# Performance work log

Measured on AMD Instinct MI355X. Metric: run time of the kernel, lower is better.

## Reference

```python
import jax, jax.numpy as jnp
import numpy as np

INF = 1000000000000000.0  # 1e15, matches the TF source

B, H, S, D = 4, 16, 1024, 64


def setup_inputs() -> dict:
    key = jax.random.key(0)
    kq, kk, kv, kp = jax.random.split(key, 4)
    q = jax.random.normal(kq, (B, H, S, D), dtype=jnp.float32)
    k = jax.random.normal(kk, (B, H, S, D), dtype=jnp.float32)
    v = jax.random.normal(kv, (B, H, S, D), dtype=jnp.float32)
    # pad_mask: 1 = masked-out key position, broadcast over heads and queries
    pad_mask = jax.random.randint(kp, (B, 1, 1, S), 0, 2, dtype=jnp.int32)
    # look_ahead_mask: 1 above the diagonal (future positions masked)
    look_ahead_mask = jnp.triu(jnp.ones((S, S), dtype=jnp.int32), k=1)[None, None]
    return {"q": q, "k": k, "v": v, "pad_mask": pad_mask,
            "look_ahead_mask": look_ahead_mask}


def reference(q, k, v, pad_mask, look_ahead_mask):
    d_model = jnp.float32(q.shape[3])
    # scores: (B, H, Sq, Sk)
    score_logits = jnp.einsum("bhqd,bhkd->bhqk", q, k) / jnp.sqrt(d_model)
    if pad_mask is not None:
        score_logits = score_logits + pad_mask.astype(jnp.float32) * (-INF)
    if look_ahead_mask is not None:
        score_logits = score_logits + look_ahead_mask.astype(jnp.float32) * (-INF)
    attention_weights = jax.nn.softmax(score_logits, axis=-1)
    context_vector = jnp.einsum("bhqk,bhkd->bhqd", attention_weights, v)
    return (context_vector, attention_weights)
```

## Files before the change

kernel.cpp:

```cpp
#include <hip/hip_runtime.h>
#include <stdint.h>

#define S 1024
#define D 64
#define TQ 16
#define KT 128
#define NKT 8
#define NEG (-1e15f)
#define SCALE 0.125f

#define WB_STRIDE 1048
#define QS_STRIDE 72

typedef __bf16 bf16x8 __attribute__((ext_vector_type(8)));
typedef float f32x4 __attribute__((ext_vector_type(4)));
typedef unsigned short ushort_t;

__device__ __forceinline__ unsigned short f2b(float f) {
  union { float f; uint32_t u; } c; c.f = f;
  uint32_t u = c.u;
  return (unsigned short)((u + 0x7fffu + ((u >> 16) & 1u)) >> 16);
}
__device__ __forceinline__ float b2f(uint32_t u) {
  union { uint32_t u; float f; } c; c.u = u << 16;
  return c.f;
}

__global__ __launch_bounds__(256) void prep_k_kernel(
    const float* __restrict__ Kg, ushort_t* __restrict__ Kb)
{
  const size_t idx = ((size_t)blockIdx.x * 256 + threadIdx.x) * 8;
  float4 a = *(const float4*)(Kg + idx);
  float4 b = *(const float4*)(Kg + idx + 4);
  ushort_t tmp[8];
  tmp[0]=f2b(a.x); tmp[1]=f2b(a.y); tmp[2]=f2b(a.z); tmp[3]=f2b(a.w);
  tmp[4]=f2b(b.x); tmp[5]=f2b(b.y); tmp[6]=f2b(b.z); tmp[7]=f2b(b.w);
  *(uint4*)(Kb + idx) = *(const uint4*)tmp;
}

__global__ __launch_bounds__(256) void prep_vt_kernel(
    const float* __restrict__ Vg, ushort_t* __restrict__ Vt)
{
  __shared__ __align__(16) ushort_t lvt[D * QS_STRIDE];
  const int t = threadIdx.x;
  const int bh = blockIdx.x >> 4;
  const int j0 = (blockIdx.x & 15) << 6;

  {
    const int j = t >> 2, sd = (t & 3) << 4;
    const float* src = Vg + ((size_t)bh * S + j0 + j) * D + sd;
#pragma unroll
    for (int c = 0; c < 4; ++c) {
      float4 f = *(const float4*)(src + (c << 2));
      lvt[(sd + (c << 2) + 0) * QS_STRIDE + j] = f2b(f.x);
      lvt[(sd + (c << 2) + 1) * QS_STRIDE + j] = f2b(f.y);
      lvt[(sd + (c << 2) + 2) * QS_STRIDE + j] = f2b(f.z);
      lvt[(sd + (c << 2) + 3) * QS_STRIDE + j] = f2b(f.w);
    }
  }
  __syncthreads();
  {
    const int d = t >> 2, sj = (t & 3) << 4;
    ushort_t tmp[16];
#pragma unroll
    for (int c = 0; c < 4; ++c)
      *(ushort4*)&tmp[c << 2] = *(const ushort4*)&lvt[d * QS_STRIDE + sj + (c << 2)];
    ushort_t* dst = Vt + ((size_t)bh * D + d) * S + j0 + sj;
    *(uint4*)dst = *(const uint4*)&tmp[0];
    *(uint4*)(dst + 8) = *(const uint4*)&tmp[8];
  }
}

__global__ __launch_bounds__(512, 6) void attn_kernel(
    const float* __restrict__ Qg, const ushort_t* __restrict__ Kb,
    const ushort_t* __restrict__ Vtb, const int* __restrict__ PADg,
    float* __restrict__ OCTX, float* __restrict__ OW)
{
  __shared__ __align__(16) ushort_t wb[TQ * WB_STRIDE];

  const int t  = threadIdx.x;
  const int w  = t >> 6;
  const int l  = t & 63;
  const int la = l & 15;
  const int lb = l >> 4;
  const int blk = blockIdx.x;
  const int bh  = blk >> 6;
  const int qt  = blk & 63;
  const int qr0 = qt << 4;

  const size_t head = (size_t)bh * S * D;
  const int* pp = PADg + (size_t)(bh >> 4) * S;

  bf16x8 aq0, aq1;
  {
    const float* qrow = Qg + head + (size_t)(qr0 + la) * D + (lb << 3);
    float4 q00 = *(const float4*)(qrow);
    float4 q01 = *(const float4*)(qrow + 4);
    float4 q10 = *(const float4*)(qrow + 32);
    float4 q11 = *(const float4*)(qrow + 36);
    ushort_t a0[8], a1[8];
    a0[0]=f2b(q00.x); a0[1]=f2b(q00.y); a0[2]=f2b(q00.z); a0[3]=f2b(q00.w);
    a0[4]=f2b(q01.x); a0[5]=f2b(q01.y); a0[6]=f2b(q01.z); a0[7]=f2b(q01.w);
    a1[0]=f2b(q10.x); a1[1]=f2b(q10.y); a1[2]=f2b(q10.z); a1[3]=f2b(q10.w);
    a1[4]=f2b(q11.x); a1[5]=f2b(q11.y); a1[6]=f2b(q11.z); a1[7]=f2b(q11.w);
    aq0 = *(const bf16x8*)a0;
    aq1 = *(const bf16x8*)a1;
  }

  {
    const ushort_t* kcol = Kb + head + (size_t)((w << 4) + la) * D + (lb << 3);
#pragma unroll
    for (int kt = 0; kt < NKT; ++kt) {
      const ushort_t* kr = kcol + (size_t)(kt * KT) * D;
      f32x4 acc = {0.f, 0.f, 0.f, 0.f};
      bf16x8 b0 = *(const bf16x8*)(kr);
      acc = __builtin_amdgcn_mfma_f32_16x16x32_bf16(aq0, b0, acc, 0, 0, 0);
      bf16x8 b1 = *(const bf16x8*)(kr + 32);
      acc = __builtin_amdgcn_mfma_f32_16x16x32_bf16(aq1, b1, acc, 0, 0, 0);
#pragma unroll
      for (int i = 0; i < 4; ++i)
        wb[((lb << 2) + i) * WB_STRIDE + kt * KT + (w << 4) + la] = f2b(acc[i]);
    }
  }
  __syncthreads();

#pragma unroll
  for (int rr = 0; rr < 2; ++rr) {
    const int r  = (w << 1) + rr;
    const int qr = qr0 + r;
    float lg[16];
    float m = -3.0e38f;
#pragma unroll
    for (int ii = 0; ii < 8; ++ii) {
      const int j = (l << 1) + (ii << 7);
      uint32_t pr = *(const uint32_t*)&wb[r * WB_STRIDE + j];
      int2 pv = *(const int2*)&pp[j];
      float l0 = b2f(pr & 0xffffu) * SCALE + (pv.x ? NEG : 0.0f) + ((j     > qr) ? NEG : 0.0f);
      float l1 = b2f(pr >> 16)     * SCALE + (pv.y ? NEG : 0.0f) + ((j + 1 > qr) ? NEG : 0.0f);
      lg[2 * ii] = l0; lg[2 * ii + 1] = l1;
      m = fmaxf(m, fmaxf(l0, l1));
    }
#pragma unroll
    for (int off = 32; off > 0; off >>= 1) m = fmaxf(m, __shfl_xor(m, off, 64));
    float sum = 0.f;
#pragma unroll
    for (int x = 0; x < 16; ++x) { lg[x] = __expf(lg[x] - m); sum += lg[x]; }
#pragma unroll
    for (int off = 32; off > 0; off >>= 1) sum += __shfl_xor(sum, off, 64);
    const float inv = 1.0f / sum;
    float* orow = OW + (size_t)(bh * S + qr) * S;
#pragma unroll
    for (int ii = 0; ii < 8; ++ii) {
      const int j = (l << 1) + (ii << 7);
      float w0 = lg[2 * ii] * inv, w1 = lg[2 * ii + 1] * inv;
      *(uint32_t*)&wb[r * WB_STRIDE + j] = ((uint32_t)f2b(w1) << 16) | (uint32_t)f2b(w0);
      unsigned long long uw = ((unsigned long long)__float_as_uint(w1) << 32)
                            | (unsigned long long)__float_as_uint(w0);
      __builtin_nontemporal_store(uw, (unsigned long long*)&orow[j]);
    }
  }
  __syncthreads();

  const int jh = w >> 2;
  const int d0 = (w & 3) << 4;
  f32x4 cacc = {0.f, 0.f, 0.f, 0.f};
  {
    const ushort_t* vrow = Vtb + (size_t)bh * D * S + (size_t)(d0 + la) * S
                          + jh * 64 + (lb << 3);
#pragma unroll
    for (int kt = 0; kt < NKT; ++kt) {
#pragma unroll
      for (int ks = 0; ks < 2; ++ks) {
        const int jt = jh * 64 + ks * 32;
        bf16x8 af = *(const bf16x8*)&wb[la * WB_STRIDE + kt * KT + jt + (lb << 3)];
        bf16x8 bf = *(const bf16x8*)(vrow + kt * KT + ks * 32);
        cacc = __builtin_amdgcn_mfma_f32_16x16x32_bf16(af, bf, cacc, 0, 0, 0);
      }
    }
  }
  __syncthreads();

  float* pbuf = (float*)wb;
  if (w >= 4) {
#pragma unroll
    for (int i = 0; i < 4; ++i)
      pbuf[(w - 4) * 320 + ((lb << 2) + i) * 20 + la] = cacc[i];
  }
  __syncthreads();
  if (w < 4) {
#pragma unroll
    for (int i = 0; i < 4; ++i) {
      const int qrow = (lb << 2) + i;
      __builtin_nontemporal_store(
          cacc[i] + pbuf[w * 320 + qrow * 20 + la],
          &OCTX[((size_t)(bh * S) + qr0 + qrow) * D + d0 + la]);
    }
  }
}

extern "C" void kernel_launch(void* const* d_in, const int* in_sizes, int n_in,
                              void* d_out, int out_size, void* d_ws, size_t ws_size,
                              hipStream_t stream) {
  const float* q   = (const float*)d_in[0];
  const float* k   = (const float*)d_in[1];
  const float* v   = (const float*)d_in[2];
  const int*   pad = (const int*)d_in[3];
  float* ctx  = (float*)d_out;
  float* wout = (float*)d_out + (size_t)4 * 16 * S * D;

  ushort_t* Kb  = (ushort_t*)d_ws;
  ushort_t* Vtb = (ushort_t*)d_ws + (size_t)4 * 16 * S * D;

  prep_k_kernel <<<dim3(2048), dim3(256), 0, stream>>>(k, Kb);
  prep_vt_kernel<<<dim3(1024), dim3(256), 0, stream>>>(v, Vtb);
  attn_kernel   <<<dim3(4096), dim3(512), 0, stream>>>(q, Kb, Vtb, pad, ctx, wout);
}
```

Before: 437.9 us.

## Remap blocks across heads and software-pipeline K and V loads with dual accumulators

Remaps the block index so consecutive hardware blocks are spread across eight heads, which is meant to change how the XCDs share L2 across K/V data. Adds explicit register prefetching of K fragments three tiles ahead in the QK^T loop. Adds prefetching of V and LDS weight fragments in the PV loop, with two alternating MFMA accumulators to break the dependency chain. The cost is higher register pressure, which could hurt occupancy under the 512x6 launch bounds.

```diff
diff --git a/kernel.cpp b/kernel.cpp
--- a/kernel.cpp
+++ b/kernel.cpp
@@ -83,10 +83,12 @@
   const int l  = t & 63;
   const int la = l & 15;
   const int lb = l >> 4;
-  const int blk = blockIdx.x;
-  const int bh  = blk >> 6;
-  const int qt  = blk & 63;
-  const int qr0 = qt << 4;
+
+  const int hwblk = blockIdx.x;
+  const int slot  = hwblk >> 3;
+  const int bh    = ((hwblk & 7) << 3) + (slot >> 6);
+  const int qt    = slot & 63;
+  const int qr0   = qt << 4;
 
   const size_t head = (size_t)bh * S * D;
   const int* pp = PADg + (size_t)(bh >> 4) * S;
@@ -108,19 +110,26 @@
   }
 
   {
-    const ushort_t* kcol = Kb + head + (size_t)((w << 4) + la) * D + (lb << 3);
+    const ushort_t* kbase = Kb + head + (size_t)((w << 4) + la) * D + (lb << 3);
+    bf16x8 k0[3], k1[3];
+#define LOADK(KTI, SL) do { \
+      const ushort_t* kr_ = kbase + (size_t)((KTI) * KT) * D; \
+      k0[SL] = *(const bf16x8*)(kr_); \
+      k1[SL] = *(const bf16x8*)(kr_ + 32); } while (0)
+    LOADK(0, 0); LOADK(1, 1); LOADK(2, 2);
 #pragma unroll
     for (int kt = 0; kt < NKT; ++kt) {
-      const ushort_t* kr = kcol + (size_t)(kt * KT) * D;
+      const int s = kt % 3;
+      bf16x8 c0 = k0[s], c1 = k1[s];
+      if (kt + 3 < NKT) LOADK(kt + 3, s);
       f32x4 acc = {0.f, 0.f, 0.f, 0.f};
-      bf16x8 b0 = *(const bf16x8*)(kr);
-      acc = __builtin_amdgcn_mfma_f32_16x16x32_bf16(aq0, b0, acc, 0, 0, 0);
-      bf16x8 b1 = *(const bf16x8*)(kr + 32);
-      acc = __builtin_amdgcn_mfma_f32_16x16x32_bf16(aq1, b1, acc, 0, 0, 0);
+      acc = __builtin_amdgcn_mfma_f32_16x16x32_bf16(aq0, c0, acc, 0, 0, 0);
+      acc = __builtin_amdgcn_mfma_f32_16x16x32_bf16(aq1, c1, acc, 0, 0, 0);
 #pragma unroll
       for (int i = 0; i < 4; ++i)
         wb[((lb << 2) + i) * WB_STRIDE + kt * KT + (w << 4) + la] = f2b(acc[i]);
     }
+#undef LOADK
   }
   __syncthreads();
 
@@ -163,20 +172,31 @@
 
   const int jh = w >> 2;
   const int d0 = (w & 3) << 4;
-  f32x4 cacc = {0.f, 0.f, 0.f, 0.f};
+  f32x4 cacc;
   {
     const ushort_t* vrow = Vtb + (size_t)bh * D * S + (size_t)(d0 + la) * S
                           + jh * 64 + (lb << 3);
-#pragma unroll
-    for (int kt = 0; kt < NKT; ++kt) {
-#pragma unroll
-      for (int ks = 0; ks < 2; ++ks) {
-        const int jt = jh * 64 + ks * 32;
-        bf16x8 af = *(const bf16x8*)&wb[la * WB_STRIDE + kt * KT + jt + (lb << 3)];
-        bf16x8 bf = *(const bf16x8*)(vrow + kt * KT + ks * 32);
-        cacc = __builtin_amdgcn_mfma_f32_16x16x32_bf16(af, bf, cacc, 0, 0, 0);
-      }
-    }
+    const ushort_t* wrow = &wb[la * WB_STRIDE + jh * 64 + (lb << 3)];
+    bf16x8 vv[3], aa[2];
+#define LOADV(ST, SL) do { \
+      vv[SL] = *(const bf16x8*)(vrow + ((ST) >> 1) * KT + ((ST) & 1) * 32); } while (0)
+#define LOADA(ST, SL) do { \
+      aa[SL] = *(const bf16x8*)(wrow + ((ST) >> 1) * KT + ((ST) & 1) * 32); } while (0)
+    LOADV(0, 0); LOADV(1, 1); LOADV(2, 2);
+    LOADA(0, 0); LOADA(1, 1);
+    f32x4 ca = {0.f, 0.f, 0.f, 0.f}, cb = {0.f, 0.f, 0.f, 0.f};
+#pragma unroll
+    for (int st = 0; st < 16; ++st) {
+      bf16x8 av = aa[st & 1];
+      bf16x8 bv = vv[st % 3];
+      if (st + 2 < 16) LOADA(st + 2, st & 1);
+      if (st + 3 < 16) LOADV(st + 3, st % 3);
+      if (st & 1) cb = __builtin_amdgcn_mfma_f32_16x16x32_bf16(av, bv, cb, 0, 0, 0);
+      else        ca = __builtin_amdgcn_mfma_f32_16x16x32_bf16(av, bv, ca, 0, 0, 0);
+    }
+    cacc = ca + cb;
+#undef LOADV
+#undef LOADA
   }
   __syncthreads();
 
```

Result: no change. 438.1 us (+0.1%).

## Prefetch K/V fragments into registers, swizzle block order, use LDS-only barriers

Applied to the files above, without the earlier changes.

Loads all K fragments into registers before the QK MFMAs, and issues the V fragment loads before the softmax so their latency overlaps with softmax work. Pad mask values are loaded once into registers instead of once per row. Blocks are remapped so consecutive hardware block IDs are spread across heads. The PV accumulation is split into two independent chains, and __syncthreads is replaced by barriers that wait only on LDS counters, so outstanding global stores are not drained. Holding the prefetched fragments raises register use, and launch bounds drop from 6 to 4 waves per SIMD to make room.

```diff
diff --git a/kernel.cpp b/kernel.cpp
--- a/kernel.cpp
+++ b/kernel.cpp
@@ -24,6 +24,12 @@
 __device__ __forceinline__ float b2f(uint32_t u) {
   union { uint32_t u; float f; } c; c.u = u << 16;
   return c.f;
+}
+
+__device__ __forceinline__ void barrier_lds_only() {
+  asm volatile("s_waitcnt lgkmcnt(0)" ::: "memory");
+  __builtin_amdgcn_s_barrier();
+  __builtin_amdgcn_sched_barrier(0);
 }
 
 __global__ __launch_bounds__(256) void prep_k_kernel(
@@ -71,7 +77,7 @@
   }
 }
 
-__global__ __launch_bounds__(512, 6) void attn_kernel(
+__global__ __launch_bounds__(512, 4) void attn_kernel(
     const float* __restrict__ Qg, const ushort_t* __restrict__ Kb,
     const ushort_t* __restrict__ Vtb, const int* __restrict__ PADg,
     float* __restrict__ OCTX, float* __restrict__ OW)
@@ -83,13 +89,24 @@
   const int l  = t & 63;
   const int la = l & 15;
   const int lb = l >> 4;
-  const int blk = blockIdx.x;
-  const int bh  = blk >> 6;
-  const int qt  = blk & 63;
-  const int qr0 = qt << 4;
+
+  const int hwblk = blockIdx.x;
+  const int slot  = hwblk >> 3;
+  const int bh    = ((hwblk & 7) << 3) + (slot >> 6);
+  const int qt    = slot & 63;
+  const int qr0   = qt << 4;
 
   const size_t head = (size_t)bh * S * D;
   const int* pp = PADg + (size_t)(bh >> 4) * S;
+
+  float padf[16];
+#pragma unroll
+  for (int ii = 0; ii < 8; ++ii) {
+    const int j = (l << 1) + (ii << 7);
+    int2 pv = *(const int2*)&pp[j];
+    padf[2 * ii]     = pv.x ? NEG : 0.0f;
+    padf[2 * ii + 1] = pv.y ? NEG : 0.0f;
+  }
 
   bf16x8 aq0, aq1;
   {
@@ -108,21 +125,33 @@
   }
 
   {
-    const ushort_t* kcol = Kb + head + (size_t)((w << 4) + la) * D + (lb << 3);
+    const ushort_t* kbase = Kb + head + (size_t)((w << 4) + la) * D + (lb << 3);
+    bf16x8 kf[16];
+#pragma unroll
+    for (int st = 0; st < 16; ++st)
+      kf[st] = *(const bf16x8*)(kbase + (size_t)(st >> 1) * (KT * D) + (st & 1) * 32);
+    __builtin_amdgcn_sched_barrier(0);
 #pragma unroll
     for (int kt = 0; kt < NKT; ++kt) {
-      const ushort_t* kr = kcol + (size_t)(kt * KT) * D;
       f32x4 acc = {0.f, 0.f, 0.f, 0.f};
-      bf16x8 b0 = *(const bf16x8*)(kr);
-      acc = __builtin_amdgcn_mfma_f32_16x16x32_bf16(aq0, b0, acc, 0, 0, 0);
-      bf16x8 b1 = *(const bf16x8*)(kr + 32);
-      acc = __builtin_amdgcn_mfma_f32_16x16x32_bf16(aq1, b1, acc, 0, 0, 0);
+      acc = __builtin_amdgcn_mfma_f32_16x16x32_bf16(aq0, kf[2 * kt],     acc, 0, 0, 0);
+      acc = __builtin_amdgcn_mfma_f32_16x16x32_bf16(aq1, kf[2 * kt + 1], acc, 0, 0, 0);
 #pragma unroll
       for (int i = 0; i < 4; ++i)
         wb[((lb << 2) + i) * WB_STRIDE + kt * KT + (w << 4) + la] = f2b(acc[i]);
     }
   }
   __syncthreads();
+
+  const int jh = w >> 2;
+  const int d0 = (w & 3) << 4;
+  const ushort_t* vrow = Vtb + (size_t)bh * (D * S) + (size_t)(d0 + la) * S
+                        + jh * 64 + (lb << 3);
+  bf16x8 vf[16];
+#pragma unroll
+  for (int st = 0; st < 16; ++st)
+    vf[st] = *(const bf16x8*)(vrow + (st >> 1) * KT + (st & 1) * 32);
+  __builtin_amdgcn_sched_barrier(0);
 
 #pragma unroll
   for (int rr = 0; rr < 2; ++rr) {
@@ -134,9 +163,8 @@
     for (int ii = 0; ii < 8; ++ii) {
       const int j = (l << 1) + (ii << 7);
       uint32_t pr = *(const uint32_t*)&wb[r * WB_STRIDE + j];
-      int2 pv = *(const int2*)&pp[j];
-      float l0 = b2f(pr & 0xffffu) * SCALE + (pv.x ? NEG : 0.0f) + ((j     > qr) ? NEG : 0.0f);
-      float l1 = b2f(pr >> 16)     * SCALE + (pv.y ? NEG : 0.0f) + ((j + 1 > qr) ? NEG : 0.0f);
+      float l0 = b2f(pr & 0xffffu) * SCALE + padf[2 * ii]     + ((j     > qr) ? NEG : 0.0f);
+      float l1 = b2f(pr >> 16)     * SCALE + padf[2 * ii + 1] + ((j + 1 > qr) ? NEG : 0.0f);
       lg[2 * ii] = l0; lg[2 * ii + 1] = l1;
       m = fmaxf(m, fmaxf(l0, l1));
     }
@@ -159,26 +187,21 @@
       __builtin_nontemporal_store(uw, (unsigned long long*)&orow[j]);
     }
   }
-  __syncthreads();
-
-  const int jh = w >> 2;
-  const int d0 = (w & 3) << 4;
-  f32x4 cacc = {0.f, 0.f, 0.f, 0.f};
-  {
-    const ushort_t* vrow = Vtb + (size_t)bh * D * S + (size_t)(d0 + la) * S
-                          + jh * 64 + (lb << 3);
-#pragma unroll
-    for (int kt = 0; kt < NKT; ++kt) {
-#pragma unroll
-      for (int ks = 0; ks < 2; ++ks) {
-        const int jt = jh * 64 + ks * 32;
-        bf16x8 af = *(const bf16x8*)&wb[la * WB_STRIDE + kt * KT + jt + (lb << 3)];
-        bf16x8 bf = *(const bf16x8*)(vrow + kt * KT + ks * 32);
-        cacc = __builtin_amdgcn_mfma_f32_16x16x32_bf16(af, bf, cacc, 0, 0, 0);
-      }
-    }
-  }
-  __syncthreads();
+  barrier_lds_only();
+
+  f32x4 cacc;
+  {
+    const ushort_t* wrow = &wb[la * WB_STRIDE + jh * 64 + (lb << 3)];
+    f32x4 ca = {0.f, 0.f, 0.f, 0.f}, cb = {0.f, 0.f, 0.f, 0.f};
+#pragma unroll
+    for (int st = 0; st < 16; ++st) {
+      bf16x8 av = *(const bf16x8*)(wrow + (st >> 1) * KT + (st & 1) * 32);
+      if (st & 1) cb = __builtin_amdgcn_mfma_f32_16x16x32_bf16(av, vf[st], cb, 0, 0, 0);
+      else        ca = __builtin_amdgcn_mfma_f32_16x16x32_bf16(av, vf[st], ca, 0, 0, 0);
+    }
+    cacc = ca + cb;
+  }
+  barrier_lds_only();
 
   float* pbuf = (float*)wb;
   if (w >= 4) {
@@ -186,7 +209,7 @@
     for (int i = 0; i < 4; ++i)
       pbuf[(w - 4) * 320 + ((lb << 2) + i) * 20 + la] = cacc[i];
   }
-  __syncthreads();
+  barrier_lds_only();
   if (w < 4) {
 #pragma unroll
     for (int i = 0; i < 4; ++i) {
```

Measured after the change: 436.3 us. Within noise of the previous version (-0.4%).

## Stage K and V tiles through LDS with register prefetch and XCD-aware block mapping

Applied to the files above, without the earlier changes.

K and V^T tiles are now loaded cooperatively and coalesced into a shared LDS buffer, one tile at a time. The next tile is prefetched into registers while the current tile is consumed by MFMA, replacing per-wave strided global loads. Block indices are remapped so that consecutive hardware blocks, which are spread across XCDs, group heads onto the same XCD to improve L2 reuse of K/V. Barriers wait only on LDS counters, so outstanding global stores and loads are not drained. The cost is extra barriers per tile, more LDS use that may reduce occupancy, and added register pressure.

```diff
diff --git a/kernel.cpp b/kernel.cpp
--- a/kernel.cpp
+++ b/kernel.cpp
@@ -10,6 +10,8 @@
 #define SCALE 0.125f
 
 #define WB_STRIDE 1048
+#define KB_STRIDE 72
+#define VT_STRIDE 136
 #define QS_STRIDE 72
 
 typedef __bf16 bf16x8 __attribute__((ext_vector_type(8)));
@@ -24,6 +26,12 @@
 __device__ __forceinline__ float b2f(uint32_t u) {
   union { uint32_t u; float f; } c; c.u = u << 16;
   return c.f;
+}
+
+__device__ __forceinline__ void barrier_lds_only() {
+  asm volatile("s_waitcnt lgkmcnt(0)" ::: "memory");
+  __builtin_amdgcn_s_barrier();
+  __builtin_amdgcn_sched_barrier(0);
 }
 
 __global__ __launch_bounds__(256) void prep_k_kernel(
@@ -77,16 +85,19 @@
     float* __restrict__ OCTX, float* __restrict__ OW)
 {
   __shared__ __align__(16) ushort_t wb[TQ * WB_STRIDE];
+  __shared__ __align__(16) ushort_t ub[KT * KB_STRIDE];
 
   const int t  = threadIdx.x;
   const int w  = t >> 6;
   const int l  = t & 63;
   const int la = l & 15;
   const int lb = l >> 4;
-  const int blk = blockIdx.x;
-  const int bh  = blk >> 6;
-  const int qt  = blk & 63;
-  const int qr0 = qt << 4;
+
+  const int hwblk = blockIdx.x;
+  const int slot  = hwblk >> 3;
+  const int bh    = ((hwblk & 7) << 3) + (slot >> 6);
+  const int qt    = slot & 63;
+  const int qr0   = qt << 4;
 
   const size_t head = (size_t)bh * S * D;
   const int* pp = PADg + (size_t)(bh >> 4) * S;
@@ -108,21 +119,37 @@
   }
 
   {
-    const ushort_t* kcol = Kb + head + (size_t)((w << 4) + la) * D + (lb << 3);
-#pragma unroll
+    const int krow = t >> 2, koff = (t & 3) << 4;
+    const ushort_t* ksrc = Kb + head + (size_t)krow * D + koff;
+    ushort_t* kdst = &ub[krow * KB_STRIDE + koff];
+    uint4 kra = *(const uint4*)(ksrc);
+    uint4 krb = *(const uint4*)(ksrc + 8);
     for (int kt = 0; kt < NKT; ++kt) {
-      const ushort_t* kr = kcol + (size_t)(kt * KT) * D;
+      *(uint4*)kdst = kra;
+      *(uint4*)(kdst + 8) = krb;
+      barrier_lds_only();
+      if (kt + 1 < NKT) {
+        const ushort_t* nsrc = ksrc + (size_t)(kt + 1) * (KT * D);
+        kra = *(const uint4*)(nsrc);
+        krb = *(const uint4*)(nsrc + 8);
+      }
+      const int j0 = w << 4;
       f32x4 acc = {0.f, 0.f, 0.f, 0.f};
-      bf16x8 b0 = *(const bf16x8*)(kr);
+      bf16x8 b0 = *(const bf16x8*)&ub[(j0 + la) * KB_STRIDE + (lb << 3)];
       acc = __builtin_amdgcn_mfma_f32_16x16x32_bf16(aq0, b0, acc, 0, 0, 0);
-      bf16x8 b1 = *(const bf16x8*)(kr + 32);
+      bf16x8 b1 = *(const bf16x8*)&ub[(j0 + la) * KB_STRIDE + 32 + (lb << 3)];
       acc = __builtin_amdgcn_mfma_f32_16x16x32_bf16(aq1, b1, acc, 0, 0, 0);
 #pragma unroll
       for (int i = 0; i < 4; ++i)
-        wb[((lb << 2) + i) * WB_STRIDE + kt * KT + (w << 4) + la] = f2b(acc[i]);
-    }
-  }
-  __syncthreads();
+        wb[((lb << 2) + i) * WB_STRIDE + kt * KT + j0 + la] = f2b(acc[i]);
+      barrier_lds_only();
+    }
+  }
+
+  const int vrow = t >> 3, voff = (t & 7) << 4;
+  const ushort_t* vsrc = Vtb + (size_t)bh * (D * S) + (size_t)vrow * S + voff;
+  uint4 vra = *(const uint4*)(vsrc);
+  uint4 vrb = *(const uint4*)(vsrc + 8);
 
 #pragma unroll
   for (int rr = 0; rr < 2; ++rr) {
@@ -159,34 +186,38 @@
       __builtin_nontemporal_store(uw, (unsigned long long*)&orow[j]);
     }
   }
-  __syncthreads();
+  barrier_lds_only();
 
   const int jh = w >> 2;
   const int d0 = (w & 3) << 4;
+  ushort_t* vdst = &ub[vrow * VT_STRIDE + voff];
   f32x4 cacc = {0.f, 0.f, 0.f, 0.f};
-  {
-    const ushort_t* vrow = Vtb + (size_t)bh * D * S + (size_t)(d0 + la) * S
-                          + jh * 64 + (lb << 3);
-#pragma unroll
-    for (int kt = 0; kt < NKT; ++kt) {
-#pragma unroll
-      for (int ks = 0; ks < 2; ++ks) {
-        const int jt = jh * 64 + ks * 32;
-        bf16x8 af = *(const bf16x8*)&wb[la * WB_STRIDE + kt * KT + jt + (lb << 3)];
-        bf16x8 bf = *(const bf16x8*)(vrow + kt * KT + ks * 32);
-        cacc = __builtin_amdgcn_mfma_f32_16x16x32_bf16(af, bf, cacc, 0, 0, 0);
-      }
-    }
-  }
-  __syncthreads();
-
-  float* pbuf = (float*)wb;
+  for (int kt = 0; kt < NKT; ++kt) {
+    *(uint4*)vdst = vra;
+    *(uint4*)(vdst + 8) = vrb;
+    barrier_lds_only();
+    if (kt + 1 < NKT) {
+      const ushort_t* nv = vsrc + (kt + 1) * KT;
+      vra = *(const uint4*)(nv);
+      vrb = *(const uint4*)(nv + 8);
+    }
+#pragma unroll
+    for (int ks = 0; ks < 2; ++ks) {
+      const int jt = jh * 64 + ks * 32;
+      bf16x8 af = *(const bf16x8*)&wb[la * WB_STRIDE + kt * KT + jt + (lb << 3)];
+      bf16x8 bf = *(const bf16x8*)&ub[(d0 + la) * VT_STRIDE + jt + (lb << 3)];
+      cacc = __builtin_amdgcn_mfma_f32_16x16x32_bf16(af, bf, cacc, 0, 0, 0);
+    }
+    barrier_lds_only();
+  }
+
+  float* pbuf = (float*)ub;
   if (w >= 4) {
 #pragma unroll
     for (int i = 0; i < 4; ++i)
       pbuf[(w - 4) * 320 + ((lb << 2) + i) * 20 + la] = cacc[i];
   }
-  __syncthreads();
+  barrier_lds_only();
   if (w < 4) {
 #pragma unroll
     for (int i = 0; i < 4; ++i) {
```

After: 390.4 us. 10.8% less time.
